# Performance work log

Hardware: AMD Instinct MI355X
Metric: run time of the kernel (lower is better)

Reference implementation:

```python
import jax, jax.numpy as jnp
import numpy as np

N, D, K = 10000, 784, 16          # nodes, input feat dim, num_neighbors
E = N * (K - 1)                   # edges
H = 128                           # hidden width in all MLPs
SIZES = [784, 128, 2]             # node_sizes


def setup_inputs() -> dict:
    key = jax.random.key(0)
    ks = jax.random.split(key, 24)
    w = lambda k, shape: jax.random.normal(k, shape, jnp.float32) * 0.02
    inp = {
        "x": jax.random.normal(ks[0], (N, D), jnp.float32),
        "edge_attr": jax.random.uniform(ks[1], (E, 1), jnp.float32),
        "idxs": jax.random.randint(ks[2], (N, K - 1), 0, N, dtype=jnp.int32),
    }
    # Layer 1: in=784, msg_size=784, out=128
    inp["l1_msg_w1"] = w(ks[3], (D + 1, H));      inp["l1_msg_b1"] = jnp.zeros((H,), jnp.float32)
    inp["l1_msg_w2"] = w(ks[4], (H, D));          inp["l1_msg_b2"] = jnp.zeros((D,), jnp.float32)
    inp["l1_node_w1"] = w(ks[5], (D + D, H));     inp["l1_node_b1"] = jnp.zeros((H,), jnp.float32)
    inp["l1_node_w2"] = w(ks[6], (H, 128));       inp["l1_node_b2"] = jnp.zeros((128,), jnp.float32)
    # Layer 2: in=128, msg_size=128, out=2
    inp["l2_msg_w1"] = w(ks[7], (128 + 1, H));    inp["l2_msg_b1"] = jnp.zeros((H,), jnp.float32)
    inp["l2_msg_w2"] = w(ks[8], (H, 128));        inp["l2_msg_b2"] = jnp.zeros((128,), jnp.float32)
    inp["l2_node_w1"] = w(ks[9], (128 + 128, H)); inp["l2_node_b1"] = jnp.zeros((H,), jnp.float32)
    inp["l2_node_w2"] = w(ks[10], (H, 2));        inp["l2_node_b2"] = jnp.zeros((2,), jnp.float32)
    return inp


def _mlp(x, w1, b1, w2, b2):
    return jax.nn.relu(x @ w1 + b1) @ w2 + b2


def _node_layer(x, src, edge_attr,
                mw1, mb1, mw2, mb2, nw1, nb1, nw2, nb2):
    # message over edges: cat(x[src], edge_attr) -> MLP   [E, msg_size]
    msg = _mlp(jnp.concatenate([x[src], edge_attr], axis=1), mw1, mb1, mw2, mb2)
    # scatter_mean by src index (faithful to the original, which uses index=src)
    sums = jax.ops.segment_sum(msg, src, num_segments=N)
    cnt = jax.ops.segment_sum(jnp.ones((src.shape[0], 1), msg.dtype), src, num_segments=N)
    agg = jnp.where(cnt > 0, sums / jnp.maximum(cnt, 1.0), 0.0)
    # node update: cat(x, agg_msg) -> MLP
    return _mlp(jnp.concatenate([x, agg], axis=1), nw1, nb1, nw2, nb2)


def reference(x, edge_attr, idxs,
              l1_msg_w1, l1_msg_b1, l1_msg_w2, l1_msg_b2,
              l1_node_w1, l1_node_b1, l1_node_w2, l1_node_b2,
              l2_msg_w1, l2_msg_b1, l2_msg_w2, l2_msg_b2,
              l2_node_w1, l2_node_b1, l2_node_w2, l2_node_b2):
    src = idxs.reshape(-1)  # [E]; dst is unused by the original message computation
    h = _node_layer(x, src, edge_attr,
                    l1_msg_w1, l1_msg_b1, l1_msg_w2, l1_msg_b2,
                    l1_node_w1, l1_node_b1, l1_node_w2, l1_node_b2)
    proj = _node_layer(h, src, edge_attr,
                       l2_msg_w1, l2_msg_b1, l2_msg_w2, l2_msg_b2,
                       l2_node_w1, l2_node_b1, l2_node_w2, l2_node_b2)  # [N, 2]
    # vectorized per-neighbor squared distances (replaces the nested python loop)
    neigh = proj[idxs]                                   # [N, K-1, 2]
    d = jnp.sum((proj[:, None, :] - neigh) ** 2, axis=-1)  # [N, K-1]
    return d.reshape(-1, 1)                              # [N*(K-1), 1]
```

## Files before the change

kernel.cpp:

```cpp
#include <hip/hip_runtime.h>

#define N_NODES 10000
#define E_EDGES 150000
#define KNB     15
#define EBLOCKS 587
#define GEMMB   1252
#define KPAD    800
#define PLSTR   204800

typedef unsigned short u16;
typedef __bf16 bf16x8 __attribute__((ext_vector_type(8)));
typedef float  f32x4  __attribute__((ext_vector_type(4)));

__device__ __forceinline__ void split3(float a, u16& h, u16& m, u16& l) {
    unsigned u = __float_as_uint(a);
    unsigned t = u + 0x7FFFu + ((u >> 16) & 1u);
    h = (u16)(t >> 16);
    float r1 = a - __uint_as_float(t & 0xFFFF0000u);
    unsigned u1 = __float_as_uint(r1);
    m = (u16)(u1 >> 16);
    float r2 = r1 - __uint_as_float(u1 & 0xFFFF0000u);
    l = (u16)(__float_as_uint(r2) >> 16);
}

__device__ __forceinline__ void gl_lds16(const u16* g, u16* l) {
    __builtin_amdgcn_global_load_lds(
        (const __attribute__((address_space(1))) unsigned int*)(g),
        (__attribute__((address_space(3))) unsigned int*)(l),
        16, 0, 0);
}

__global__ void count_kernel(const int* __restrict__ idxs, int* __restrict__ cnt, int e) {
    int i = blockIdx.x * blockDim.x + threadIdx.x;
    if (i < e) atomicAdd(&cnt[idxs[i]], 1);
}

__device__ __forceinline__
void gemm_tile2(const float* __restrict__ A, int K,
                const float* __restrict__ Blo, const float* __restrict__ Bhi, int ldB,
                float* __restrict__ C, int ldC, int M,
                int rowBlk, int colBlk) {
    __shared__ float As2[16][34];
    __shared__ float Bs2[16][64];
    int tid = threadIdx.x;
    int tn  = tid & 15, tm = tid >> 4;
    int arow = tid >> 3, acB = (tid & 7) << 1;
    int brow = tid >> 4, bcol = (tid & 15) << 2;
    int rowBase = rowBlk * 32, colBase = colBlk * 64;

    bool half = (Bhi != nullptr) && (colBase >= 128);
    const float* B = half ? Bhi : Blo;
    int bj = colBase - (half ? 128 : 0) + bcol;

    float2 av; float4 bv;
    auto loadA = [&](int k0, float2& dst) {
        int gr = rowBase + arow;
        if (gr < M) dst = *(const float2*)(A + (size_t)gr * K + k0 + acB);
        else { dst.x = dst.y = 0.f; }
    };
    auto loadB = [&](int k0, float4& dst) {
        dst = *(const float4*)(B + (size_t)(k0 + brow) * ldB + bj);
    };
    loadA(0, av); loadB(0, bv);

    float acc[2][4] = {};
    for (int k0 = 0; k0 < K; k0 += 16) {
        __syncthreads();
        As2[acB + 0][arow] = av.x; As2[acB + 1][arow] = av.y;
        *(float4*)&Bs2[brow][bcol] = bv;
        __syncthreads();
        if (k0 + 16 < K) { loadA(k0 + 16, av); loadB(k0 + 16, bv); }
#pragma unroll
        for (int k = 0; k < 16; ++k) {
            float4 b = *(const float4*)&Bs2[k][tn << 2];
            float2 a = *(const float2*)&As2[k][tm << 1];
            acc[0][0] = fmaf(a.x, b.x, acc[0][0]); acc[0][1] = fmaf(a.x, b.y, acc[0][1]);
            acc[0][2] = fmaf(a.x, b.z, acc[0][2]); acc[0][3] = fmaf(a.x, b.w, acc[0][3]);
            acc[1][0] = fmaf(a.y, b.x, acc[1][0]); acc[1][1] = fmaf(a.y, b.y, acc[1][1]);
            acc[1][2] = fmaf(a.y, b.z, acc[1][2]); acc[1][3] = fmaf(a.y, b.w, acc[1][3]);
        }
    }
#pragma unroll
    for (int i = 0; i < 2; ++i) {
        int row = rowBase + tm * 2 + i;
        if (row >= M) continue;
#pragma unroll
        for (int j = 0; j < 4; ++j)
            C[(size_t)row * ldC + colBase + (tn << 2) + j] = acc[i][j];
    }
}

__global__ __launch_bounds__(256)
void scanfold_kernel(const float* __restrict__ mw2, const float* __restrict__ mb2,
                     const float* __restrict__ nw1, const float* __restrict__ nb2,
                     const float* __restrict__ nw2,
                     const float* __restrict__ m2w1, const float* __restrict__ m2b1,
                     const float* __restrict__ m2w2, const float* __restrict__ m2b2,
                     const float* __restrict__ n2w1, const float* __restrict__ n2b1,
                     float* __restrict__ M1, float* __restrict__ M2,
                     float* __restrict__ WH,
                     float* __restrict__ v1, float* __restrict__ v2,
                     float* __restrict__ bu2, float* __restrict__ bx2,
                     const int* __restrict__ cnt, int* __restrict__ eoff,
                     float* __restrict__ maskv, int* __restrict__ fillc,
                     const float* __restrict__ mw1, u16* __restrict__ Bt) {
    int b = blockIdx.x;
    if (b >= 41) {
        __shared__ float Lt[KPAD][17];
        int b2 = b - 41;
        int colBase = b2 * 16;
        const float* S = (colBase < 128) ? mw1 : nw1;
        int sc = colBase & 127;
        int tid = threadIdx.x;
        for (int i = 0; i < 50; ++i) {
            int row = (tid >> 4) + i * 16;
            Lt[row][tid & 15] = (row < 784) ? S[(size_t)row * 128 + sc + (tid & 15)] : 0.f;
        }
        __syncthreads();
        int col = tid >> 4, o = tid & 15;
        size_t dbase = (size_t)(colBase + col) * KPAD;
        for (int o2 = o; o2 < 100; o2 += 16) {
            u16 hs[8], ms[8], ls[8];
#pragma unroll
            for (int e = 0; e < 8; ++e) split3(Lt[o2 * 8 + e][col], hs[e], ms[e], ls[e]);
            auto pk = [](const u16* s) {
                uint4 v;
                v.x = s[0] | ((unsigned)s[1] << 16); v.y = s[2] | ((unsigned)s[3] << 16);
                v.z = s[4] | ((unsigned)s[5] << 16); v.w = s[6] | ((unsigned)s[7] << 16);
                return v;
            };
            *(uint4*)(Bt +           dbase + o2 * 8) = pk(hs);
            *(uint4*)(Bt + PLSTR   + dbase + o2 * 8) = pk(ms);
            *(uint4*)(Bt + 2*PLSTR + dbase + o2 * 8) = pk(ls);
        }
        return;
    }
    if (b == 0) {
        __shared__ int ssum[256];
        int tid = threadIdx.x;
        const int CH = 40;
        int base = tid * CH;
        int v[CH]; int s = 0;
#pragma unroll
        for (int q = 0; q < CH; ++q) {
            int i = base + q;
            v[q] = (i < N_NODES) ? cnt[i] : 0;
            s += v[q];
        }
        ssum[tid] = s;
        __syncthreads();
        for (int off = 1; off < 256; off <<= 1) {
            int t = (tid >= off) ? ssum[tid - off] : 0;
            __syncthreads();
            ssum[tid] += t;
            __syncthreads();
        }
        int ex = ssum[tid] - s;
#pragma unroll
        for (int q = 0; q < CH; ++q) {
            int i = base + q;
            if (i < N_NODES) {
                eoff[i]  = ex;
                maskv[i] = (v[q] > 0) ? 1.f : 0.f;
                fillc[i] = 0;
                ex += v[q];
            }
        }
        return;
    }
    b -= 1;
    if (b < 8) {
        gemm_tile2(mw2, 784, nw1 + 784 * 128, nullptr, 128, M1, 128, 128, b >> 1, b & 1);
    } else if (b < 16) {
        int t = b - 8;
        gemm_tile2(m2w2, 128, n2w1 + 128 * 128, nullptr, 128, M2, 128, 128, t >> 1, t & 1);
    } else if (b < 32) {
        int t = b - 16;
        gemm_tile2(nw2, 128, m2w1, n2w1, 128, WH, 256, 128, t >> 2, t & 3);
    } else {
        __shared__ float red[256];
        int t  = (b - 32) >> 1;
        int j  = ((b - 32) & 1) * 64 + (threadIdx.x & 63);
        int kq = threadIdx.x >> 6;
        const float* bvec; const float* Bv; const float* add; float* out; int Kv;
        if (t == 0)      { bvec = mb2;  Bv = nw1 + 784 * 128;  add = nullptr; out = v1;  Kv = 784; }
        else if (t == 1) { bvec = m2b2; Bv = n2w1 + 128 * 128; add = nullptr; out = v2;  Kv = 128; }
        else if (t == 2) { bvec = nb2;  Bv = m2w1;             add = m2b1;    out = bu2; Kv = 128; }
        else             { bvec = nb2;  Bv = n2w1;             add = n2b1;    out = bx2; Kv = 128; }
        float acc = 0.f;
        for (int k = kq; k < Kv; k += 4) acc = fmaf(bvec[k], Bv[k * 128 + j], acc);
        red[threadIdx.x] = acc;
        __syncthreads();
        if (threadIdx.x < 64) {
            float tot = red[threadIdx.x] + red[threadIdx.x + 64] +
                        red[threadIdx.x + 128] + red[threadIdx.x + 192];
            out[j] = tot + (add ? add[j] : 0.f);
        }
    }
}

#define MF(a, b, c) __builtin_amdgcn_mfma_f32_16x16x32_bf16((a), (b), (c), 0, 0, 0)

__device__ __forceinline__
void gemm_mfma(const float* __restrict__ A, const u16* __restrict__ Bt,
               const float* __restrict__ biasLo, const float* __restrict__ biasHi,
               const float* __restrict__ vhi, const float* __restrict__ rowmask,
               float* __restrict__ C, int gb) {
    __shared__ u16 As[3][2][64][8];
    __shared__ u16 Bs[2][3][4][64][8];
    const int tid  = threadIdx.x;
    const int lane = tid & 63, w = tid >> 6;
    const int rb = gb >> 2, cbq = gb & 3;
    const int rowBase = rb * 32, colBase = cbq * 64;
    const bool hi = cbq >= 2;
    u16* const AsB = &As[0][0][0][0];
    u16* const BsB = &Bs[0][0][0][0][0];

    const int srf   = w & 1;
    const int chunk = ((w >> 1) << 2) + (lane >> 4);
    const int aoff  = chunk << 2;
    int arow = rowBase + srf * 16 + (lane & 15);
    if (arow > N_NODES - 1) arow = N_NODES - 1;
    const float* Ap = A + (size_t)arow * 784;
    u16* aDst = AsB + srf * 512 + (((lane & 15) + ((chunk >> 1) << 4)) << 3)
                    + ((chunk & 1) << 2);

#define BSRC(c) ((size_t)((c) >> 2) * PLSTR + \
                 (size_t)(colBase + (((c) & 3) << 4) + (lane & 15)) * KPAD + \
                 ((lane >> 4) << 3))
    const int c0 = w * 3, c1 = w * 3 + 1, c2 = w * 3 + 2;
    const u16* bsrc0 = Bt + BSRC(c0);
    const u16* bsrc1 = Bt + BSRC(c1);
    const u16* bsrc2 = Bt + BSRC(c2);
    const int bo0 = c0 * 512, bo1 = c1 * 512, bo2 = c2 * 512;
#undef BSRC

    float4 av;
    ushort4 a3h, a3m, a3l;

#define ALOAD(k0) { int kk = (k0) + aoff; \
    if (kk < 784) av = *(const float4*)(Ap + kk); \
    else { av.x = av.y = av.z = av.w = 0.f; } }
#define ASPLIT() { u16 h, m, l; \
    split3(av.x, h, m, l); a3h.x = h; a3m.x = m; a3l.x = l; \
    split3(av.y, h, m, l); a3h.y = h; a3m.y = m; a3l.y = l; \
    split3(av.z, h, m, l); a3h.z = h; a3m.z = m; a3l.z = l; \
    split3(av.w, h, m, l); a3h.w = h; a3m.w = m; a3l.w = l; }

    f32x4 acc0 = {0.f, 0.f, 0.f, 0.f};
    f32x4 acc1 = acc0;

    const u16* aFr = AsB + (lane << 3);

    ALOAD(0) ASPLIT()
    gl_lds16(bsrc0, BsB + bo0);
    gl_lds16(bsrc1, BsB + bo1);
    gl_lds16(bsrc2, BsB + bo2);

    for (int t = 0; t < 25; ++t) {
        __syncthreads();
        *(ushort4*)(aDst)        = a3h;
        *(ushort4*)(aDst + 1024) = a3m;
        *(ushort4*)(aDst + 2048) = a3l;
        __syncthreads();
        if (t < 24) {
            const int kn = (t + 1) << 5;
            ALOAD(kn)
            u16* bb = BsB + (((t + 1) & 1) ? 6144 : 0);
            gl_lds16(bsrc0 + kn, bb + bo0);
            gl_lds16(bsrc1 + kn, bb + bo1);
            gl_lds16(bsrc2 + kn, bb + bo2);
        }
        const u16* bFr = BsB + ((t & 1) ? 6144 : 0) + (w << 9) + (lane << 3);
        {
            bf16x8 a0h = *(const bf16x8*)(aFr);
            bf16x8 a1h = *(const bf16x8*)(aFr + 512);
            bf16x8 a0m = *(const bf16x8*)(aFr + 1024);
            bf16x8 a1m = *(const bf16x8*)(aFr + 1536);
            bf16x8 a0l = *(const bf16x8*)(aFr + 2048);
            bf16x8 a1l = *(const bf16x8*)(aFr + 2560);
            bf16x8 bh  = *(const bf16x8*)(bFr);
            bf16x8 bm  = *(const bf16x8*)(bFr + 2048);
            bf16x8 bl  = *(const bf16x8*)(bFr + 4096);
            acc0 = MF(a0h, bh, acc0); acc1 = MF(a1h, bh, acc1);
            acc0 = MF(a0m, bh, acc0); acc1 = MF(a1m, bh, acc1);
            acc0 = MF(a0l, bh, acc0); acc1 = MF(a1l, bh, acc1);
            acc0 = MF(a0h, bm, acc0); acc1 = MF(a1h, bm, acc1);
            acc0 = MF(a0m, bm, acc0); acc1 = MF(a1m, bm, acc1);
            acc0 = MF(a0h, bl, acc0); acc1 = MF(a1h, bl, acc1);
        }
        if (t < 24) ASPLIT()
    }
#undef ALOAD
#undef ASPLIT

    const float* bias = hi ? biasHi : biasLo;
#define EPI(rf, ACC) { \
        const int col = colBase + w * 16 + (lane & 15); \
        const int cj  = col & 127; \
        const float bb = bias[cj]; \
        const float vh = hi ? vhi[cj] : 0.f; \
        const int rbase = rowBase + (rf) * 16 + ((lane >> 4) << 2); \
        _Pragma("unroll") \
        for (int rr = 0; rr < 4; ++rr) { \
            int row = rbase + rr; \
            if (row < N_NODES) { \
                float v = ACC[rr] + bb; \
                if (hi) v = fmaf(rowmask[row], vh, v); \
                C[(size_t)row * 256 + col] = v; \
            } } }
    EPI(0, acc0) EPI(1, acc1)
#undef EPI
}

__global__ __launch_bounds__(256, 5)
void fillgemm_kernel(const int* __restrict__ idxs, const float* __restrict__ ea,
                     const int* __restrict__ eoff, int* __restrict__ fillc,
                     float* __restrict__ eas,
                     const float* __restrict__ A, const u16* __restrict__ Bt,
                     const float* __restrict__ biasLo, const float* __restrict__ biasHi,
                     const float* __restrict__ vhi, const float* __restrict__ rowmask,
                     float* __restrict__ C) {
    int gb = blockIdx.x;
    if (gb < GEMMB) {
        gemm_mfma(A, Bt, biasLo, biasHi, vhi, rowmask, C, gb);
        return;
    }
    int i = (gb - GEMMB) * 256 + threadIdx.x;
    if (i < E_EDGES) {
        int s = idxs[i];
        int p = atomicAdd(&fillc[s], 1);
        eas[eoff[s] + p] = ea[i];
    }
}

__global__ __launch_bounds__(512, 4)
void tail16_kernel(const float* __restrict__ UX1, const float* __restrict__ w1last,
                   const float* __restrict__ eas, const int* __restrict__ eoff,
                   const int* __restrict__ cnt, const float* __restrict__ maskv,
                   const float* __restrict__ M1, const float* __restrict__ WH,
                   const float* __restrict__ bu2, const float* __restrict__ bx2,
                   const float* __restrict__ v2,
                   const float* __restrict__ w2last, const float* __restrict__ M2,
                   const float* __restrict__ pw, const float* __restrict__ pb,
                   float* __restrict__ UX2, float* __restrict__ proj) {
    __shared__ float Bs[16][264];
    __shared__ float mhT[128][18];
    __shared__ float ts[16][132];
    __shared__ float ebuf[1024];
    int rowBase = blockIdx.x * 16;
    int tid = threadIdx.x;
    int tr  = tid >> 5;
    int tn  = tid & 31;
    int c4  = tn << 2;

    auto msg_phase = [&](const float* __restrict__ U, const float* __restrict__ wl) {
        int d = tid & 127, grp = tid >> 7;
        float w = wl[d];
        float uu[4], sum[4];
        int es[4], ec[4];
#pragma unroll
        for (int it = 0; it < 4; ++it) {
            int n  = rowBase + it * 4 + grp;
            ec[it] = cnt[n];
            es[it] = eoff[n];
            uu[it] = U[(size_t)n * 256 + d];
            sum[it] = 0.f;
        }
        int ebase = eoff[rowBase];
        int eend  = (rowBase + 16 < N_NODES) ? eoff[rowBase + 16] : E_EDGES;
        for (int w0 = ebase; w0 < eend; w0 += 1024) {
            int wlen = min(1024, eend - w0);
            __syncthreads();
            for (int q = tid; q < wlen; q += 512) ebuf[q] = eas[w0 + q];
            __syncthreads();
#pragma unroll
            for (int it = 0; it < 4; ++it) {
                int lo = max(es[it], w0), hiE = min(es[it] + ec[it], w0 + wlen);
                for (int e = lo; e < hiE; ++e)
                    sum[it] += fmaxf(fmaf(ebuf[e - w0], w, uu[it]), 0.f);
            }
        }
#pragma unroll
        for (int it = 0; it < 4; ++it)
            mhT[d][it * 4 + grp] = (ec[it] > 0) ? sum[it] / (float)ec[it] : 0.f;
    };

    msg_phase(UX1, w1last);

    {
        float a0 = 0.f, a1 = 0.f, a2 = 0.f, a3 = 0.f;
        float4 bv = *(const float4*)(M1 + (size_t)tr * 128 + c4);
        for (int k0 = 0; k0 < 128; k0 += 16) {
            __syncthreads();
            *(float4*)&Bs[tr][c4] = bv;
            __syncthreads();
            if (k0 + 16 < 128)
                bv = *(const float4*)(M1 + (size_t)(k0 + 16 + tr) * 128 + c4);
#pragma unroll
            for (int k = 0; k < 16; ++k) {
                float a = mhT[k0 + k][tr];
                float4 b = *(const float4*)&Bs[k][c4];
                a0 = fmaf(a, b.x, a0); a1 = fmaf(a, b.y, a1);
                a2 = fmaf(a, b.z, a2); a3 = fmaf(a, b.w, a3);
            }
        }
        int row = rowBase + tr;
        float4 xn = *(const float4*)(UX1 + (size_t)row * 256 + 128 + c4);
        float4 o;
        o.x = fmaxf(a0 + xn.x, 0.f);
        o.y = fmaxf(a1 + xn.y, 0.f);
        o.z = fmaxf(a2 + xn.z, 0.f);
        o.w = fmaxf(a3 + xn.w, 0.f);
        *(float4*)&ts[tr][c4] = o;
    }

    {
        float u0 = 0.f, u1 = 0.f, u2 = 0.f, u3 = 0.f;
        float x0 = 0.f, x1 = 0.f, x2 = 0.f, x3 = 0.f;
        int c8 = tn << 3;
        float4 bva = *(const float4*)(WH + (size_t)tr * 256 + c8);
        float4 bvb = *(const float4*)(WH + (size_t)tr * 256 + c8 + 4);
        for (int k0 = 0; k0 < 128; k0 += 16) {
            __syncthreads();
            *(float4*)&Bs[tr][c8]     = bva;
            *(float4*)&Bs[tr][c8 + 4] = bvb;
            __syncthreads();
            if (k0 + 16 < 128) {
                bva = *(const float4*)(WH + (size_t)(k0 + 16 + tr) * 256 + c8);
                bvb = *(const float4*)(WH + (size_t)(k0 + 16 + tr) * 256 + c8 + 4);
            }
#pragma unroll
            for (int k = 0; k < 16; ++k) {
                float a = ts[tr][k0 + k];
                float4 b0 = *(const float4*)&Bs[k][c4];
                float4 b1 = *(const float4*)&Bs[k][c4 + 128];
                u0 = fmaf(a, b0.x, u0); u1 = fmaf(a, b0.y, u1);
                u2 = fmaf(a, b0.z, u2); u3 = fmaf(a, b0.w, u3);
                x0 = fmaf(a, b1.x, x0); x1 = fmaf(a, b1.y, x1);
                x2 = fmaf(a, b1.z, x2); x3 = fmaf(a, b1.w, x3);
            }
        }
        int row = rowBase + tr;
        float rm = maskv[row];
        float4 o0, o1;
        o0.x = u0 + bu2[c4 + 0]; o0.y = u1 + bu2[c4 + 1];
        o0.z = u2 + bu2[c4 + 2]; o0.w = u3 + bu2[c4 + 3];
        o1.x = fmaf(rm, v2[c4 + 0], x0 + bx2[c4 + 0]);
        o1.y = fmaf(rm, v2[c4 + 1], x1 + bx2[c4 + 1]);
        o1.z = fmaf(rm, v2[c4 + 2], x2 + bx2[c4 + 2]);
        o1.w = fmaf(rm, v2[c4 + 3], x3 + bx2[c4 + 3]);
        float* orow = UX2 + (size_t)row * 256;
        *(float4*)(orow + c4)       = o0;
        *(float4*)(orow + 128 + c4) = o1;
    }
    __syncthreads();

    msg_phase(UX2, w2last);

    {
        float a0 = 0.f, a1 = 0.f, a2 = 0.f, a3 = 0.f;
        float4 bv = *(const float4*)(M2 + (size_t)tr * 128 + c4);
        for (int k0 = 0; k0 < 128; k0 += 16) {
            __syncthreads();
            *(float4*)&Bs[tr][c4] = bv;
            __syncthreads();
            if (k0 + 16 < 128)
                bv = *(const float4*)(M2 + (size_t)(k0 + 16 + tr) * 128 + c4);
#pragma unroll
            for (int k = 0; k < 16; ++k) {
                float a = mhT[k0 + k][tr];
                float4 b = *(const float4*)&Bs[k][c4];
                a0 = fmaf(a, b.x, a0); a1 = fmaf(a, b.y, a1);
                a2 = fmaf(a, b.z, a2); a3 = fmaf(a, b.w, a3);
            }
        }
        int row = rowBase + tr;
        float4 xn = *(const float4*)(UX2 + (size_t)row * 256 + 128 + c4);
        float t0 = fmaxf(a0 + xn.x, 0.f);
        float t1 = fmaxf(a1 + xn.y, 0.f);
        float t2 = fmaxf(a2 + xn.z, 0.f);
        float t3 = fmaxf(a3 + xn.w, 0.f);
        float pp0 = fmaf(t3, pw[2*(c4+3)],   fmaf(t2, pw[2*(c4+2)],   fmaf(t1, pw[2*(c4+1)],   t0 * pw[2*c4])));
        float pp1 = fmaf(t3, pw[2*(c4+3)+1], fmaf(t2, pw[2*(c4+2)+1], fmaf(t1, pw[2*(c4+1)+1], t0 * pw[2*c4+1])));
        for (int off = 16; off > 0; off >>= 1) {
            pp0 += __shfl_xor(pp0, off, 64);
            pp1 += __shfl_xor(pp1, off, 64);
        }
        if (tn == 0) {
            proj[2 * row]     = pp0 + pb[0];
            proj[2 * row + 1] = pp1 + pb[1];
        }
    }
}

__global__ void dist_kernel(const float* __restrict__ proj, const int* __restrict__ idxs,
                            float* __restrict__ out, int e) {
    int i = blockIdx.x * blockDim.x + threadIdx.x;
    if (i >= e) return;
    int n = i / KNB;
    int m = idxs[i];
    float2 pn = *(const float2*)(proj + 2 * n);
    float2 pm = *(const float2*)(proj + 2 * m);
    float dx = pn.x - pm.x;
    float dy = pn.y - pm.y;
    out[i] = dx * dx + dy * dy;
}

extern "C" void kernel_launch(void* const* d_in, const int* in_sizes, int n_in,
                              void* d_out, int out_size, void* d_ws, size_t ws_size,
                              hipStream_t stream) {
    (void)in_sizes; (void)n_in; (void)out_size; (void)ws_size;
    const float* x    = (const float*)d_in[0];
    const float* eatt = (const float*)d_in[1];
    const int*   idxs = (const int*)d_in[2];
    const float* mw1  = (const float*)d_in[3];
    const float* mb1  = (const float*)d_in[4];
    const float* mw2  = (const float*)d_in[5];
    const float* mb2  = (const float*)d_in[6];
    const float* nw1  = (const float*)d_in[7];
    const float* nb1  = (const float*)d_in[8];
    const float* nw2  = (const float*)d_in[9];
    const float* nb2  = (const float*)d_in[10];
    const float* m2w1 = (const float*)d_in[11];
    const float* m2b1 = (const float*)d_in[12];
    const float* m2w2 = (const float*)d_in[13];
    const float* m2b2 = (const float*)d_in[14];
    const float* n2w1 = (const float*)d_in[15];
    const float* n2b1 = (const float*)d_in[16];
    const float* n2w2 = (const float*)d_in[17];
    const float* n2b2 = (const float*)d_in[18];
    float* out = (float*)d_out;

    float* fws   = (float*)d_ws;
    float* UX1   = fws;
    float* UX2   = fws + 2560000;
    float* proj  = fws + 5120000;
    float* maskv = fws + 5140000;
    float* eas   = fws + 5150016;
    float* M1    = fws + 5300016;
    float* M2    = fws + 5316400;
    float* WH    = fws + 5332784;
    float* v1    = fws + 5365552;
    float* v2    = fws + 5365680;
    float* bu2   = fws + 5365808;
    float* bx2   = fws + 5365936;
    int*   cnt   = (int*)(fws + 5366064);
    int*   fillc = cnt + N_NODES;
    int*   eoff  = fillc + N_NODES;
    u16*   Bt    = (u16*)(fws + 2560000);

    hipMemsetAsync(cnt, 0, N_NODES * sizeof(int), stream);
    count_kernel<<<EBLOCKS, 256, 0, stream>>>(idxs, cnt, E_EDGES);

    scanfold_kernel<<<57, 256, 0, stream>>>(mw2, mb2, nw1, nb2, nw2,
                                            m2w1, m2b1, m2w2, m2b2, n2w1, n2b1,
                                            M1, M2, WH, v1, v2, bu2, bx2,
                                            cnt, eoff, maskv, fillc, mw1, Bt);

    fillgemm_kernel<<<GEMMB + EBLOCKS, 256, 0, stream>>>(
        idxs, eatt, eoff, fillc, eas,
        x, Bt, mb1, nb1, v1, maskv, UX1);

    tail16_kernel<<<625, 512, 0, stream>>>(UX1, mw1 + 784 * 128, eas, eoff, cnt, maskv,
                                           M1, WH, bu2, bx2, v2,
                                           m2w1 + 128 * 128, M2,
                                           n2w2, n2b2,
                                           UX2, proj);

    dist_kernel<<<EBLOCKS, 256, 0, stream>>>(proj, idxs, out, E_EDGES);
}
```

Measured before the change: 251.0 us.

## Double-buffer A tile in LDS to remove one barrier per k-step

The A-operand LDS tile is now double-buffered like B, so the split bf16 pieces for the next k-step are written into the alternate buffer and the global load runs two steps ahead. This drops the second __syncthreads per iteration and overlaps the A load and split with MFMA work. It costs extra LDS and registers, so launch bounds drop from 5 to 4 waves per SIMD, which may reduce occupancy.

After: 257.0 us. 1.02x slower.

```diff
diff --git a/kernel.cpp b/kernel.cpp
--- a/kernel.cpp
+++ b/kernel.cpp
@@ -206,14 +206,14 @@
                const float* __restrict__ biasLo, const float* __restrict__ biasHi,
                const float* __restrict__ vhi, const float* __restrict__ rowmask,
                float* __restrict__ C, int gb) {
-    __shared__ u16 As[3][2][64][8];
+    __shared__ u16 As[2][3][2][64][8];
     __shared__ u16 Bs[2][3][4][64][8];
     const int tid  = threadIdx.x;
     const int lane = tid & 63, w = tid >> 6;
     const int rb = gb >> 2, cbq = gb & 3;
     const int rowBase = rb * 32, colBase = cbq * 64;
     const bool hi = cbq >= 2;
-    u16* const AsB = &As[0][0][0][0];
+    u16* const AsB = &As[0][0][0][0][0];
     u16* const BsB = &Bs[0][0][0][0][0];
 
     const int srf   = w & 1;
@@ -222,8 +222,8 @@
     int arow = rowBase + srf * 16 + (lane & 15);
     if (arow > N_NODES - 1) arow = N_NODES - 1;
     const float* Ap = A + (size_t)arow * 784;
-    u16* aDst = AsB + srf * 512 + (((lane & 15) + ((chunk >> 1) << 4)) << 3)
-                    + ((chunk & 1) << 2);
+    const int aOff = srf * 512 + (((lane & 15) + ((chunk >> 1) << 4)) << 3)
+                   + ((chunk & 1) << 2);
 
 #define BSRC(c) ((size_t)((c) >> 2) * PLSTR + \
                  (size_t)(colBase + (((c) & 3) << 4) + (lane & 15)) * KPAD + \
@@ -246,42 +246,43 @@
     split3(av.y, h, m, l); a3h.y = h; a3m.y = m; a3l.y = l; \
     split3(av.z, h, m, l); a3h.z = h; a3m.z = m; a3l.z = l; \
     split3(av.w, h, m, l); a3h.w = h; a3m.w = m; a3l.w = l; }
+#define AWRITE(BUF) { u16* ab = AsB + (BUF) * 3072 + aOff; \
+    *(ushort4*)(ab)        = a3h; \
+    *(ushort4*)(ab + 1024) = a3m; \
+    *(ushort4*)(ab + 2048) = a3l; }
+#define BPREF(BUF, k0) { u16* bb = BsB + (BUF) * 6144; \
+    gl_lds16(bsrc0 + (k0), bb + bo0); \
+    gl_lds16(bsrc1 + (k0), bb + bo1); \
+    gl_lds16(bsrc2 + (k0), bb + bo2); }
 
     f32x4 acc0 = {0.f, 0.f, 0.f, 0.f};
     f32x4 acc1 = acc0;
 
-    const u16* aFr = AsB + (lane << 3);
-
     ALOAD(0) ASPLIT()
-    gl_lds16(bsrc0, BsB + bo0);
-    gl_lds16(bsrc1, BsB + bo1);
-    gl_lds16(bsrc2, BsB + bo2);
+    BPREF(0, 0)
+    AWRITE(0)
+    ALOAD(32) ASPLIT()
 
     for (int t = 0; t < 25; ++t) {
         __syncthreads();
-        *(ushort4*)(aDst)        = a3h;
-        *(ushort4*)(aDst + 1024) = a3m;
-        *(ushort4*)(aDst + 2048) = a3l;
-        __syncthreads();
+        const int nb = (t + 1) & 1;
         if (t < 24) {
-            const int kn = (t + 1) << 5;
-            ALOAD(kn)
-            u16* bb = BsB + (((t + 1) & 1) ? 6144 : 0);
-            gl_lds16(bsrc0 + kn, bb + bo0);
-            gl_lds16(bsrc1 + kn, bb + bo1);
-            gl_lds16(bsrc2 + kn, bb + bo2);
-        }
-        const u16* bFr = BsB + ((t & 1) ? 6144 : 0) + (w << 9) + (lane << 3);
+            AWRITE(nb)
+            BPREF(nb, (t + 1) << 5)
+        }
+        if (t < 23) ALOAD((t + 2) << 5)
+        const u16* aF = AsB + (t & 1) * 3072 + (lane << 3);
+        const u16* bF = BsB + (t & 1) * 6144 + (w << 9) + (lane << 3);
         {
-            bf16x8 a0h = *(const bf16x8*)(aFr);
-            bf16x8 a1h = *(const bf16x8*)(aFr + 512);
-            bf16x8 a0m = *(const bf16x8*)(aFr + 1024);
-            bf16x8 a1m = *(const bf16x8*)(aFr + 1536);
-            bf16x8 a0l = *(const bf16x8*)(aFr + 2048);
-            bf16x8 a1l = *(const bf16x8*)(aFr + 2560);
-            bf16x8 bh  = *(const bf16x8*)(bFr);
-            bf16x8 bm  = *(const bf16x8*)(bFr + 2048);
-            bf16x8 bl  = *(const bf16x8*)(bFr + 4096);
+            bf16x8 a0h = *(const bf16x8*)(aF);
+            bf16x8 a1h = *(const bf16x8*)(aF + 512);
+            bf16x8 a0m = *(const bf16x8*)(aF + 1024);
+            bf16x8 a1m = *(const bf16x8*)(aF + 1536);
+            bf16x8 a0l = *(const bf16x8*)(aF + 2048);
+            bf16x8 a1l = *(const bf16x8*)(aF + 2560);
+            bf16x8 bh  = *(const bf16x8*)(bF);
+            bf16x8 bm  = *(const bf16x8*)(bF + 2048);
+            bf16x8 bl  = *(const bf16x8*)(bF + 4096);
             acc0 = MF(a0h, bh, acc0); acc1 = MF(a1h, bh, acc1);
             acc0 = MF(a0m, bh, acc0); acc1 = MF(a1m, bh, acc1);
             acc0 = MF(a0l, bh, acc0); acc1 = MF(a1l, bh, acc1);
@@ -289,10 +290,12 @@
             acc0 = MF(a0m, bm, acc0); acc1 = MF(a1m, bm, acc1);
             acc0 = MF(a0h, bl, acc0); acc1 = MF(a1h, bl, acc1);
         }
-        if (t < 24) ASPLIT()
+        if (t < 23) ASPLIT()
     }
 #undef ALOAD
 #undef ASPLIT
+#undef AWRITE
+#undef BPREF
 
     const float* bias = hi ? biasHi : biasLo;
 #define EPI(rf, ACC) { \
@@ -313,7 +316,7 @@
 #undef EPI
 }
 
-__global__ __launch_bounds__(256, 5)
+__global__ __launch_bounds__(256, 4)
 void fillgemm_kernel(const int* __restrict__ idxs, const float* __restrict__ ea,
                      const int* __restrict__ eoff, int* __restrict__ fillc,
                      float* __restrict__ eas,
```
